# Optimization experiments

Hardware: AMD Instinct MI355X
Metric: run time of the kernel (lower is better)

## Reference

```python
import jax, jax.numpy as jnp
import numpy as np

B, N, D, H, MLP = 4, 1024, 1024, 16, 4096  # seq_len N must equal dim D; D = H * dim_head
DH = D // H
EPS = 1e-5


def layernorm(x, g, b):
    mu = jnp.mean(x, axis=-1, keepdims=True)
    var = jnp.var(x, axis=-1, keepdims=True)
    return (x - mu) * jax.lax.rsqrt(var + EPS) * g + b


def setup_inputs() -> dict:
    key = jax.random.key(0)
    ks = jax.random.split(key, 12)
    s = 0.02
    return {
        "x": jax.random.normal(ks[0], (B, N, D), jnp.float32),
        "enc_out": jax.random.normal(ks[1], (B, N, D), jnp.float32),
        # SelfAttention (heads=1, dim_head=D); weights stored (in, out) so we apply x @ W
        "sa_wq": jax.random.normal(ks[2], (D, D), jnp.float32) * s,
        "sa_wk": jax.random.normal(ks[3], (D, D), jnp.float32) * s,
        "sa_wv": jax.random.normal(ks[4], (D, D), jnp.float32) * s,
        "sa_g": jnp.ones((D,), jnp.float32),
        "sa_b": jnp.zeros((D,), jnp.float32),
        # CrossAttention
        "ca_wq": jax.random.normal(ks[5], (D, D), jnp.float32) * s,
        "ca_wk": jax.random.normal(ks[6], (D, D), jnp.float32) * s,
        "ca_wv": jax.random.normal(ks[7], (D, D), jnp.float32) * s,
        "ca_g": jnp.ones((D,), jnp.float32),
        "ca_b": jnp.zeros((D,), jnp.float32),
        # FeedForward
        "w1": jax.random.normal(ks[8], (D, MLP), jnp.float32) * s,
        "b1": jnp.zeros((MLP,), jnp.float32),
        "w2": jax.random.normal(ks[9], (MLP, D), jnp.float32) * s,
        "b2": jnp.zeros((D,), jnp.float32),
        "ff_g": jnp.ones((D,), jnp.float32),
        "ff_b": jnp.zeros((D,), jnp.float32),
    }


def reference(x, enc_out, sa_wq, sa_wk, sa_wv, sa_g, sa_b,
              ca_wq, ca_wk, ca_wv, ca_g, ca_b,
              w1, b1, w2, b2, ff_g, ff_b):
    b, n, d = x.shape
    # --- SelfAttention: heads=1, dim_head=dim -> scale = dim**-0.5 ---
    sa_scale = 1.0 / jnp.sqrt(jnp.asarray(d, x.dtype))
    q = x @ sa_wq
    k = x @ sa_wk
    v = x @ sa_wv
    dots = jnp.einsum('bid,bjd->bij', q, k) * sa_scale
    attn = jax.nn.softmax(dots, axis=-1)
    sa = jnp.einsum('bij,bjd->bid', attn, v)
    sa = layernorm(sa + x, sa_g, sa_b)

    # --- CrossAttention: Q . (K K^T) before softmax ---
    dh = d // H
    ca_scale = 1.0 / jnp.sqrt(jnp.asarray(dh, x.dtype))
    qc = sa @ ca_wq                                     # [b, n, d]; broadcast over heads
    kc = (enc_out @ ca_wk).reshape(b, n, H, dh).transpose(0, 2, 1, 3)  # [b, h, n, dh]
    vc = (enc_out @ ca_wv).reshape(b, n, H, dh).transpose(0, 2, 1, 3)
    kkt = jnp.einsum('bhid,bhjd->bhij', kc, kc) * ca_scale             # [b, h, n, n]
    dots = jnp.einsum('bid,bhjd->bhij', qc, kkt) * ca_scale            # q's d contracts kkt's last dim (n == d)
    attn = jax.nn.softmax(dots, axis=-1)
    out = jnp.einsum('bhij,bhjd->bhid', attn, vc)
    out = out.transpose(0, 2, 1, 3).reshape(b, n, d)
    ca = layernorm(out + enc_out, ca_g, ca_b)

    # --- FeedForward (dropout = identity in eval) ---
    h = jax.nn.gelu(ca @ w1 + b1, approximate=False) @ w2 + b2
    return layernorm(h + ca, ff_g, ff_b)
```

## Files before the change

kernel.cpp:

```cpp
#include <hip/hip_runtime.h>
#include <math.h>
#include <stdint.h>

typedef unsigned short u16;
typedef u16   u16x8 __attribute__((ext_vector_type(8)));
typedef __bf16 bf16x8 __attribute__((ext_vector_type(8)));
typedef float  f32x4 __attribute__((ext_vector_type(4)));

#define B_   4
#define N_   1024
#define D_   1024
#define MLP_ 4096

__device__ __forceinline__ float bf2f(u16 v) {
    unsigned u = ((unsigned)v) << 16;
    return __builtin_bit_cast(float, u);
}
__device__ __forceinline__ u16 f2bf(float f) {
    unsigned u = __builtin_bit_cast(unsigned, f);
    u += 0x7fff + ((u >> 16) & 1);
    return (u16)(u >> 16);
}
__device__ __forceinline__ bf16x8 ld8(const u16* p) {
    return __builtin_bit_cast(bf16x8, *(const u16x8*)p);
}
__device__ __forceinline__ void gll16(const u16* g, u16* l) {
    __builtin_amdgcn_global_load_lds(
        (const __attribute__((address_space(1))) unsigned int*)g,
        (__attribute__((address_space(3))) unsigned int*)l,
        16, 0, 0);
}

__global__ __launch_bounds__(256)
void f32_to_bf16_k(const float* __restrict__ in, u16* __restrict__ out, int n8)
{
    int i = blockIdx.x * 256 + threadIdx.x;
    if (i < n8) {
        f32x4 a = *(const f32x4*)&in[(long)i * 8];
        f32x4 b = *(const f32x4*)&in[(long)i * 8 + 4];
        u16x8 h;
        h[0] = f2bf(a[0]); h[1] = f2bf(a[1]); h[2] = f2bf(a[2]); h[3] = f2bf(a[3]);
        h[4] = f2bf(b[0]); h[5] = f2bf(b[1]); h[6] = f2bf(b[2]); h[7] = f2bf(b[3]);
        *(u16x8*)&out[(long)i * 8] = h;
    }
}

template<int TN, int OUTF32, int BIAS, int GELU>
__global__ __launch_bounds__(256, 2)
void gemm_a(const u16* __restrict__ A, const u16* __restrict__ Bt,
            void* __restrict__ Cv, const float* __restrict__ bias,
            float scale, int K,
            int lda, int ldb, int ldc,
            long sA, long sB, long sC)
{
    constexpr int NT = TN / 32;
    __shared__ alignas(16) u16 As[2][128 * 32];
    __shared__ alignas(16) u16 Bs[2][TN * 32];
    const int bz = blockIdx.z;
    A  += bz * sA;  Bt += bz * sB;
    char* Cp = (char*)Cv + bz * sC * (OUTF32 ? 4 : 2);
    const int m0 = blockIdx.x * 128, n0 = blockIdx.y * TN;
    const int t = threadIdx.x, lane = t & 63, w = t >> 6;
    const int wr = (w >> 1) * 64, wc = (w & 1) * (TN / 2);
    const int fr = lane & 15, fq = lane >> 4, fk = fq * 8;
    f32x4 acc[4][NT] = {};

    const int r0a = t >> 2, c0a = (t & 3) * 8;
    auto stageA = [&](u16* dst, int k0) {
        gll16(A + (long)(m0 + r0a) * lda + k0 + c0a,      dst + w * 512);
        gll16(A + (long)(m0 + 64 + r0a) * lda + k0 + c0a, dst + 2048 + w * 512);
    };
    auto stageB = [&](u16* dst, int k0) {
        gll16(Bt + (long)(n0 + r0a) * ldb + k0 + c0a, dst + w * 512);
        if (TN == 128)
            gll16(Bt + (long)(n0 + 64 + r0a) * ldb + k0 + c0a, dst + 2048 + w * 512);
    };

    stageA(As[0], 0);
    stageB(Bs[0], 0);
    int cur = 0;
    for (int k0 = 0; k0 < K; k0 += 32) {
        __syncthreads();
        if (k0 + 32 < K) {
            stageA(As[cur ^ 1], k0 + 32);
            stageB(Bs[cur ^ 1], k0 + 32);
        }
        const u16* as = As[cur];
        const u16* bs = Bs[cur];
        bf16x8 af[4], bfv[NT];
#pragma unroll
        for (int mt = 0; mt < 4; mt++) af [mt] = ld8(&as[(wr + mt * 16 + fr) * 32 + fk]);
#pragma unroll
        for (int nt = 0; nt < NT; nt++) bfv[nt] = ld8(&bs[(wc + nt * 16 + fr) * 32 + fk]);
#pragma unroll
        for (int mt = 0; mt < 4; mt++)
#pragma unroll
            for (int nt = 0; nt < NT; nt++)
                acc[mt][nt] = __builtin_amdgcn_mfma_f32_16x16x32_bf16(af[mt], bfv[nt], acc[mt][nt], 0, 0, 0);
        cur ^= 1;
    }

#pragma unroll
    for (int nt = 0; nt < NT; nt++) {
        const int col = n0 + wc + nt * 16 + fr;
        float bv = 0.f;
        if (BIAS) bv = bias[col];
#pragma unroll
        for (int mt = 0; mt < 4; mt++) {
            const int rbase = m0 + wr + mt * 16 + fq * 4;
#pragma unroll
            for (int r = 0; r < 4; r++) {
                float v = acc[mt][nt][r] * scale;
                if (BIAS) v += bv;
                if (GELU) v = 0.5f * v * (1.0f + erff(v * 0.70710678118654752f));
                long idx = (long)(rbase + r) * ldc + col;
                if (OUTF32) ((float*)Cp)[idx] = v;
                else        ((u16*) Cp)[idx] = f2bf(v);
            }
        }
    }
}

template<int INF32>
__global__ __launch_bounds__(256)
void transpose_cast(const void* __restrict__ in, u16* __restrict__ out,
                    int R, int C, long sIn, long sOut)
{
    __shared__ u16 tile[32][33];
    const char* ip = (const char*)in + (long)blockIdx.z * sIn * (INF32 ? 4 : 2);
    u16*        op = out + (long)blockIdx.z * sOut;
    const int bx = blockIdx.x * 32, by = blockIdx.y * 32;
    const int tx = threadIdx.x & 31, ty = threadIdx.x >> 5;
#pragma unroll
    for (int i = ty; i < 32; i += 8) {
        long idx = (long)(by + i) * C + bx + tx;
        tile[i][tx] = INF32 ? f2bf(((const float*)ip)[idx]) : ((const u16*)ip)[idx];
    }
    __syncthreads();
#pragma unroll
    for (int i = ty; i < 32; i += 8) op[(long)(bx + i) * R + by + tx] = tile[tx][i];
}

__global__ __launch_bounds__(256)
void softmax_1024(const float* __restrict__ in, u16* __restrict__ out)
{
    const int lane = threadIdx.x & 63, wv = threadIdx.x >> 6;
    const long row = (long)blockIdx.x * 4 + wv;
    const float* p = in + row * 1024;
    float v[16], mx = -1e30f;
#pragma unroll
    for (int i = 0; i < 16; i++) { v[i] = p[lane + i * 64]; mx = fmaxf(mx, v[i]); }
#pragma unroll
    for (int off = 32; off; off >>= 1) mx = fmaxf(mx, __shfl_xor(mx, off, 64));
    float s = 0.f;
#pragma unroll
    for (int i = 0; i < 16; i++) { v[i] = __expf(v[i] - mx); s += v[i]; }
#pragma unroll
    for (int off = 32; off; off >>= 1) s += __shfl_xor(s, off, 64);
    const float inv = 1.0f / s;
    u16* q = out + row * 1024;
#pragma unroll
    for (int i = 0; i < 16; i++) q[lane + i * 64] = f2bf(v[i] * inv);
}

template<int AF32, int RESF32, int OUTF32>
__global__ __launch_bounds__(256)
void ln_res(const void* __restrict__ Av, const void* __restrict__ Rv,
            const float* __restrict__ g, const float* __restrict__ be,
            void* __restrict__ out)
{
    const int lane = threadIdx.x & 63, wv = threadIdx.x >> 6;
    const long row = (long)blockIdx.x * 4 + wv;
    float v[16], s = 0.f;
#pragma unroll
    for (int i = 0; i < 16; i++) {
        long idx = row * 1024 + lane + i * 64;
        float a = AF32   ? ((const float*)Av)[idx] : bf2f(((const u16*)Av)[idx]);
        float r = RESF32 ? ((const float*)Rv)[idx] : bf2f(((const u16*)Rv)[idx]);
        v[i] = a + r;
        s += v[i];
    }
#pragma unroll
    for (int off = 32; off; off >>= 1) s += __shfl_xor(s, off, 64);
    const float mu = s * (1.f / 1024.f);
    float s2 = 0.f;
#pragma unroll
    for (int i = 0; i < 16; i++) { float d = v[i] - mu; s2 += d * d; }
#pragma unroll
    for (int off = 32; off; off >>= 1) s2 += __shfl_xor(s2, off, 64);
    const float rs = rsqrtf(s2 * (1.f / 1024.f) + 1e-5f);
#pragma unroll
    for (int i = 0; i < 16; i++) {
        int c = lane + i * 64;
        float o = (v[i] - mu) * rs * g[c] + be[c];
        if (OUTF32) ((float*)out)[row * 1024 + c] = o;
        else        ((u16*) out)[row * 1024 + c] = f2bf(o);
    }
}

__global__ __launch_bounds__(256, 2)
void flash_ca(const u16* __restrict__ P, const u16* __restrict__ Kc,
              const u16* __restrict__ VT, u16* __restrict__ O)
{
    __shared__ alignas(16) u16 Qs[64 * 72];
    __shared__ alignas(16) u16 Ks[64 * 72];
    __shared__ alignas(16) u16 Vs[64 * 72];
    __shared__ alignas(16) u16 Ps[64 * 72];
    const int b = blockIdx.z, h = blockIdx.y, it = blockIdx.x;
    const long base = (long)b * N_ * D_;
    const int t = threadIdx.x, lane = t & 63, w = t >> 6;
    const int fr = lane & 15, fq = lane >> 4, fk = fq * 8;

#pragma unroll
    for (int i = 0; i < 2; i++) {
        int c = i * 256 + t, row = c >> 3, col = (c & 7) * 8;
        *(u16x8*)&Qs[row * 72 + col] =
            *(const u16x8*)&P[base + (long)(it * 64 + row) * D_ + h * 64 + col];
    }
    f32x4 o[4] = {};
    float m_r[4], l_r[4];
#pragma unroll
    for (int r = 0; r < 4; r++) { m_r[r] = -1e30f; l_r[r] = 0.f; }

    for (int jt = 0; jt < 16; jt++) {
        __syncthreads();
#pragma unroll
        for (int i = 0; i < 2; i++) {
            int c = i * 256 + t, row = c >> 3, col = (c & 7) * 8;
            *(u16x8*)&Ks[row * 72 + col] =
                *(const u16x8*)&Kc[base + (long)(jt * 64 + row) * D_ + h * 64 + col];
            *(u16x8*)&Vs[row * 72 + col] =
                *(const u16x8*)&VT[base + (long)(h * 64 + row) * D_ + jt * 64 + col];
        }
        __syncthreads();

        f32x4 st[4] = {};
        {
            bf16x8 a0 = ld8(&Qs[(w * 16 + fr) * 72 + fk]);
            bf16x8 a1 = ld8(&Qs[(w * 16 + fr) * 72 + 32 + fk]);
#pragma unroll
            for (int nt = 0; nt < 4; nt++) {
                bf16x8 b0 = ld8(&Ks[(nt * 16 + fr) * 72 + fk]);
                bf16x8 b1 = ld8(&Ks[(nt * 16 + fr) * 72 + 32 + fk]);
                st[nt] = __builtin_amdgcn_mfma_f32_16x16x32_bf16(a0, b0, st[nt], 0, 0, 0);
                st[nt] = __builtin_amdgcn_mfma_f32_16x16x32_bf16(a1, b1, st[nt], 0, 0, 0);
            }
        }
        float alpha[4];
#pragma unroll
        for (int r = 0; r < 4; r++) {
            float mx = fmaxf(fmaxf(st[0][r], st[1][r]), fmaxf(st[2][r], st[3][r]));
#pragma unroll
            for (int off = 1; off < 16; off <<= 1) mx = fmaxf(mx, __shfl_xor(mx, off, 64));
            float mn = fmaxf(m_r[r], mx);
            alpha[r] = __expf(m_r[r] - mn);
            m_r[r] = mn;
        }
        float rsum[4] = {0.f, 0.f, 0.f, 0.f};
#pragma unroll
        for (int nt = 0; nt < 4; nt++)
#pragma unroll
            for (int r = 0; r < 4; r++) {
                float e = __expf(st[nt][r] - m_r[r]);
                st[nt][r] = e;
                rsum[r] += e;
            }
#pragma unroll
        for (int r = 0; r < 4; r++) {
#pragma unroll
            for (int off = 1; off < 16; off <<= 1) rsum[r] += __shfl_xor(rsum[r], off, 64);
            l_r[r] = l_r[r] * alpha[r] + rsum[r];
        }
#pragma unroll
        for (int dt = 0; dt < 4; dt++)
#pragma unroll
            for (int r = 0; r < 4; r++) o[dt][r] *= alpha[r];

#pragma unroll
        for (int nt = 0; nt < 4; nt++)
#pragma unroll
            for (int r = 0; r < 4; r++)
                Ps[(w * 16 + fq * 4 + r) * 72 + nt * 16 + fr] = f2bf(st[nt][r]);
        __asm__ volatile("s_waitcnt lgkmcnt(0)" ::: "memory");
        bf16x8 p0 = ld8(&Ps[(w * 16 + fr) * 72 + fk]);
        bf16x8 p1 = ld8(&Ps[(w * 16 + fr) * 72 + 32 + fk]);
#pragma unroll
        for (int dt = 0; dt < 4; dt++) {
            bf16x8 v0 = ld8(&Vs[(dt * 16 + fr) * 72 + fk]);
            bf16x8 v1 = ld8(&Vs[(dt * 16 + fr) * 72 + 32 + fk]);
            o[dt] = __builtin_amdgcn_mfma_f32_16x16x32_bf16(p0, v0, o[dt], 0, 0, 0);
            o[dt] = __builtin_amdgcn_mfma_f32_16x16x32_bf16(p1, v1, o[dt], 0, 0, 0);
        }
    }
#pragma unroll
    for (int dt = 0; dt < 4; dt++)
#pragma unroll
        for (int r = 0; r < 4; r++) {
            float v = o[dt][r] / l_r[r];
            O[base + (long)(it * 64 + w * 16 + fq * 4 + r) * D_ + h * 64 + dt * 16 + fr] = f2bf(v);
        }
}

extern "C" void kernel_launch(void* const* d_in, const int* in_sizes, int n_in,
                              void* d_out, int out_size, void* d_ws, size_t ws_size,
                              hipStream_t stream)
{
    const float* x     = (const float*)d_in[0];
    const float* enc   = (const float*)d_in[1];
    const float* sa_wq = (const float*)d_in[2];
    const float* sa_wk = (const float*)d_in[3];
    const float* sa_wv = (const float*)d_in[4];
    const float* sa_g  = (const float*)d_in[5];
    const float* sa_b  = (const float*)d_in[6];
    const float* ca_wq = (const float*)d_in[7];
    const float* ca_wk = (const float*)d_in[8];
    const float* ca_wv = (const float*)d_in[9];
    const float* ca_g  = (const float*)d_in[10];
    const float* ca_b  = (const float*)d_in[11];
    const float* w1    = (const float*)d_in[12];
    const float* b1    = (const float*)d_in[13];
    const float* w2    = (const float*)d_in[14];
    const float* b2    = (const float*)d_in[15];
    const float* ff_g  = (const float*)d_in[16];
    const float* ff_b  = (const float*)d_in[17];

    char* ws = (char*)d_ws;
    const size_t MB = 1ull << 20;
    u16*  qkB   = (u16*)(ws + 0 * MB);
    u16*  E     = (u16*)(ws + 0 * MB);
    u16*  h1B   = (u16*)(ws + 0 * MB);
    float* scF  = (float*)(ws + 16 * MB);
    u16*  xB    = (u16*)(ws + 32 * MB);
    u16*  encB  = (u16*)(ws + 40 * MB);
    float* h2F  = (float*)(ws + 32 * MB);
    u16*  Wsa   = (u16*)(ws + 48 * MB);
    u16*  qB    = (u16*)(ws + 48 * MB);
    u16*  calnB = (u16*)(ws + 48 * MB);
    u16*  kB    = (u16*)(ws + 56 * MB);
    u16*  w2T   = (u16*)(ws + 56 * MB);
    u16*  vTB   = (u16*)(ws + 64 * MB);
    u16*  w1T   = (u16*)(ws + 64 * MB);
    u16*  attnB = (u16*)(ws + 72 * MB);
    u16*  Wca   = (u16*)(ws + 72 * MB);

    const dim3 blk(256, 1, 1);
    const long M1 = (long)N_ * D_;
    const long M2 = 2 * M1;

    f32_to_bf16_k<<<dim3(2048, 1, 1), blk, 0, stream>>>(x,   xB,   524288);
    f32_to_bf16_k<<<dim3(2048, 1, 1), blk, 0, stream>>>(enc, encB, 524288);

    transpose_cast<1><<<dim3(32, 32, 1), blk, 0, stream>>>(sa_wq, Wsa,          1024, 1024, 0, 0);
    transpose_cast<1><<<dim3(32, 32, 1), blk, 0, stream>>>(sa_wk, Wsa + M1,     1024, 1024, 0, 0);
    transpose_cast<1><<<dim3(32, 32, 1), blk, 0, stream>>>(sa_wv, Wsa + 2 * M1, 1024, 1024, 0, 0);

    gemm_a<128,0,0,0><<<dim3(32, 16, 1), blk, 0, stream>>>(xB, Wsa, qkB, nullptr,
        1.f, 1024, 1024, 1024, 2048, 0, 0, 0);
    gemm_a<64,0,0,0><<<dim3(8, 16, 4), blk, 0, stream>>>(Wsa + 2 * M1, xB, vTB, nullptr,
        1.f, 1024, 1024, 1024, 1024, 0, M1, M1);
    gemm_a<64,1,0,0><<<dim3(8, 16, 4), blk, 0, stream>>>(qkB, qkB + 1024, scF, nullptr,
        0.03125f, 1024, 2048, 2048, 1024, M2, M2, M1);
    softmax_1024<<<dim3(1024, 1, 1), blk, 0, stream>>>(scF, attnB);
    gemm_a<64,1,0,0><<<dim3(8, 16, 4), blk, 0, stream>>>(attnB, vTB, scF, nullptr,
        1.f, 1024, 1024, 1024, 1024, M1, M1, M1);
    ln_res<1,1,0><<<dim3(1024, 1, 1), blk, 0, stream>>>(scF, x, sa_g, sa_b, E);

    transpose_cast<1><<<dim3(32, 32, 1), blk, 0, stream>>>(ca_wq, Wca,          1024, 1024, 0, 0);
    transpose_cast<1><<<dim3(32, 32, 1), blk, 0, stream>>>(ca_wk, Wca + M1,     1024, 1024, 0, 0);
    transpose_cast<1><<<dim3(32, 32, 1), blk, 0, stream>>>(ca_wv, Wca + 2 * M1, 1024, 1024, 0, 0);
    gemm_a<64,0,0,0><<<dim3(32, 16, 1), blk, 0, stream>>>(E, Wca, qB, nullptr,
        1.f, 1024, 1024, 1024, 1024, 0, 0, 0);
    gemm_a<64,0,0,0><<<dim3(32, 16, 1), blk, 0, stream>>>(encB, Wca + M1, kB, nullptr,
        1.f, 1024, 1024, 1024, 1024, 0, 0, 0);
    gemm_a<64,0,0,0><<<dim3(8, 16, 4), blk, 0, stream>>>(Wca + 2 * M1, encB, vTB, nullptr,
        1.f, 1024, 1024, 1024, 1024, 0, M1, M1);
    transpose_cast<0><<<dim3(32, 32, 4), blk, 0, stream>>>(kB, E, 1024, 1024, M1, M1);
    gemm_a<64,0,0,0><<<dim3(8, 16, 4), blk, 0, stream>>>(qB, E, attnB, nullptr,
        0.015625f, 1024, 1024, 1024, 1024, M1, M1, M1);
    flash_ca<<<dim3(16, 16, 4), blk, 0, stream>>>(attnB, kB, vTB, E);
    ln_res<0,1,0><<<dim3(1024, 1, 1), blk, 0, stream>>>(E, enc, ca_g, ca_b, calnB);

    transpose_cast<1><<<dim3(128, 32, 1), blk, 0, stream>>>(w1, w1T, 1024, 4096, 0, 0);
    transpose_cast<1><<<dim3(32, 128, 1), blk, 0, stream>>>(w2, w2T, 4096, 1024, 0, 0);
    gemm_a<128,0,1,1><<<dim3(32, 32, 1), blk, 0, stream>>>(calnB, w1T, h1B, b1,
        1.f, 1024, 1024, 1024, 4096, 0, 0, 0);
    gemm_a<64,1,1,0><<<dim3(32, 16, 1), blk, 0, stream>>>(h1B, w2T, h2F, b2,
        1.f, 4096, 4096, 4096, 1024, 0, 0, 0);
    ln_res<1,0,1><<<dim3(1024, 1, 1), blk, 0, stream>>>(h2F, calnB, ff_g, ff_b, (float*)d_out);
}
```

Before: 568.3 us.

## Double-buffer flash cross-attention with async loads and shrink GEMM M tiles

flash_ca now handles 128 query rows per block with Q held in registers, and double-buffers K/V tiles in LDS via async global-to-LDS loads so the next tile's fetch overlaps compute. It also drops the online running-max rescaling and exponentiates the raw scores, normalizing once at the end. That removes per-tile reductions and rescales but can overflow if scores are large. Separately, the GEMM gains a templated M tile, so most calls use 64x64 tiles with higher occupancy hints to put more blocks on the GPU.

```diff
diff --git a/kernel.cpp b/kernel.cpp
--- a/kernel.cpp
+++ b/kernel.cpp
@@ -45,35 +45,36 @@
     }
 }
 
-template<int TN, int OUTF32, int BIAS, int GELU>
-__global__ __launch_bounds__(256, 2)
+template<int TM, int TN, int OUTF32, int BIAS, int GELU>
+__global__ __launch_bounds__(256, 4)
 void gemm_a(const u16* __restrict__ A, const u16* __restrict__ Bt,
             void* __restrict__ Cv, const float* __restrict__ bias,
             float scale, int K,
             int lda, int ldb, int ldc,
             long sA, long sB, long sC)
 {
-    constexpr int NT = TN / 32;
-    __shared__ alignas(16) u16 As[2][128 * 32];
+    constexpr int MT = TM / 32, NT = TN / 32;
+    __shared__ alignas(16) u16 As[2][TM * 32];
     __shared__ alignas(16) u16 Bs[2][TN * 32];
     const int bz = blockIdx.z;
     A  += bz * sA;  Bt += bz * sB;
     char* Cp = (char*)Cv + bz * sC * (OUTF32 ? 4 : 2);
-    const int m0 = blockIdx.x * 128, n0 = blockIdx.y * TN;
+    const int m0 = blockIdx.x * TM, n0 = blockIdx.y * TN;
     const int t = threadIdx.x, lane = t & 63, w = t >> 6;
-    const int wr = (w >> 1) * 64, wc = (w & 1) * (TN / 2);
+    const int wr = (w >> 1) * (TM / 2), wc = (w & 1) * (TN / 2);
     const int fr = lane & 15, fq = lane >> 4, fk = fq * 8;
-    f32x4 acc[4][NT] = {};
+    f32x4 acc[MT][NT] = {};
 
     const int r0a = t >> 2, c0a = (t & 3) * 8;
     auto stageA = [&](u16* dst, int k0) {
-        gll16(A + (long)(m0 + r0a) * lda + k0 + c0a,      dst + w * 512);
-        gll16(A + (long)(m0 + 64 + r0a) * lda + k0 + c0a, dst + 2048 + w * 512);
+#pragma unroll
+        for (int p = 0; p < TM / 64; p++)
+            gll16(A + (long)(m0 + p * 64 + r0a) * lda + k0 + c0a, dst + p * 2048 + w * 512);
     };
     auto stageB = [&](u16* dst, int k0) {
-        gll16(Bt + (long)(n0 + r0a) * ldb + k0 + c0a, dst + w * 512);
-        if (TN == 128)
-            gll16(Bt + (long)(n0 + 64 + r0a) * ldb + k0 + c0a, dst + 2048 + w * 512);
+#pragma unroll
+        for (int p = 0; p < TN / 64; p++)
+            gll16(Bt + (long)(n0 + p * 64 + r0a) * ldb + k0 + c0a, dst + p * 2048 + w * 512);
     };
 
     stageA(As[0], 0);
@@ -87,13 +88,13 @@
         }
         const u16* as = As[cur];
         const u16* bs = Bs[cur];
-        bf16x8 af[4], bfv[NT];
-#pragma unroll
-        for (int mt = 0; mt < 4; mt++) af [mt] = ld8(&as[(wr + mt * 16 + fr) * 32 + fk]);
+        bf16x8 af[MT], bfv[NT];
+#pragma unroll
+        for (int mt = 0; mt < MT; mt++) af [mt] = ld8(&as[(wr + mt * 16 + fr) * 32 + fk]);
 #pragma unroll
         for (int nt = 0; nt < NT; nt++) bfv[nt] = ld8(&bs[(wc + nt * 16 + fr) * 32 + fk]);
 #pragma unroll
-        for (int mt = 0; mt < 4; mt++)
+        for (int mt = 0; mt < MT; mt++)
 #pragma unroll
             for (int nt = 0; nt < NT; nt++)
                 acc[mt][nt] = __builtin_amdgcn_mfma_f32_16x16x32_bf16(af[mt], bfv[nt], acc[mt][nt], 0, 0, 0);
@@ -106,7 +107,7 @@
         float bv = 0.f;
         if (BIAS) bv = bias[col];
 #pragma unroll
-        for (int mt = 0; mt < 4; mt++) {
+        for (int mt = 0; mt < MT; mt++) {
             const int rbase = m0 + wr + mt * 16 + fq * 4;
 #pragma unroll
             for (int r = 0; r < 4; r++) {
@@ -198,107 +199,107 @@
     }
 }
 
-__global__ __launch_bounds__(256, 2)
+__global__ __launch_bounds__(256, 3)
 void flash_ca(const u16* __restrict__ P, const u16* __restrict__ Kc,
               const u16* __restrict__ VT, u16* __restrict__ O)
 {
-    __shared__ alignas(16) u16 Qs[64 * 72];
-    __shared__ alignas(16) u16 Ks[64 * 72];
-    __shared__ alignas(16) u16 Vs[64 * 72];
-    __shared__ alignas(16) u16 Ps[64 * 72];
+    __shared__ alignas(16) u16 Ks[2][64 * 64];
+    __shared__ alignas(16) u16 Vs[2][64 * 64];
+    __shared__ alignas(16) u16 Ps[128 * 72];
     const int b = blockIdx.z, h = blockIdx.y, it = blockIdx.x;
     const long base = (long)b * N_ * D_;
     const int t = threadIdx.x, lane = t & 63, w = t >> 6;
-    const int fr = lane & 15, fq = lane >> 4, fk = fq * 8;
-
-#pragma unroll
-    for (int i = 0; i < 2; i++) {
-        int c = i * 256 + t, row = c >> 3, col = (c & 7) * 8;
-        *(u16x8*)&Qs[row * 72 + col] =
-            *(const u16x8*)&P[base + (long)(it * 64 + row) * D_ + h * 64 + col];
-    }
-    f32x4 o[4] = {};
-    float m_r[4], l_r[4];
-#pragma unroll
-    for (int r = 0; r < 4; r++) { m_r[r] = -1e30f; l_r[r] = 0.f; }
-
+    const int fr = lane & 15, fq = lane >> 4;
+
+    bf16x8 qf[2][2];
+#pragma unroll
+    for (int mt = 0; mt < 2; mt++)
+#pragma unroll
+        for (int hf = 0; hf < 2; hf++)
+            qf[mt][hf] = ld8(&P[base + (long)(it * 128 + w * 32 + mt * 16 + fr) * D_
+                                + h * 64 + hf * 32 + fq * 8]);
+
+    auto stageK = [&](int buf, int jt) {
+#pragma unroll
+        for (int p = 0; p < 2; p++)
+            gll16(Kc + base + (long)(jt * 64 + p * 32 + (t >> 3)) * D_ + h * 64 + (t & 7) * 8,
+                  &Ks[buf][p * 2048 + w * 512]);
+    };
+    auto stageV = [&](int buf, int jt) {
+#pragma unroll
+        for (int p = 0; p < 2; p++)
+            gll16(VT + base + (long)(h * 64 + p * 32 + (t >> 3)) * D_ + jt * 64 + (t & 7) * 8,
+                  &Vs[buf][p * 2048 + w * 512]);
+    };
+
+    f32x4 o[2][4] = {};
+    float l_lane[2][4] = {};
+
+    stageK(0, 0); stageV(0, 0);
+    int cur = 0;
     for (int jt = 0; jt < 16; jt++) {
         __syncthreads();
-#pragma unroll
-        for (int i = 0; i < 2; i++) {
-            int c = i * 256 + t, row = c >> 3, col = (c & 7) * 8;
-            *(u16x8*)&Ks[row * 72 + col] =
-                *(const u16x8*)&Kc[base + (long)(jt * 64 + row) * D_ + h * 64 + col];
-            *(u16x8*)&Vs[row * 72 + col] =
-                *(const u16x8*)&VT[base + (long)(h * 64 + row) * D_ + jt * 64 + col];
-        }
-        __syncthreads();
-
-        f32x4 st[4] = {};
-        {
-            bf16x8 a0 = ld8(&Qs[(w * 16 + fr) * 72 + fk]);
-            bf16x8 a1 = ld8(&Qs[(w * 16 + fr) * 72 + 32 + fk]);
-#pragma unroll
-            for (int nt = 0; nt < 4; nt++) {
-                bf16x8 b0 = ld8(&Ks[(nt * 16 + fr) * 72 + fk]);
-                bf16x8 b1 = ld8(&Ks[(nt * 16 + fr) * 72 + 32 + fk]);
-                st[nt] = __builtin_amdgcn_mfma_f32_16x16x32_bf16(a0, b0, st[nt], 0, 0, 0);
-                st[nt] = __builtin_amdgcn_mfma_f32_16x16x32_bf16(a1, b1, st[nt], 0, 0, 0);
+        if (jt + 1 < 16) { stageK(cur ^ 1, jt + 1); stageV(cur ^ 1, jt + 1); }
+        const u16* ks = Ks[cur];
+        const u16* vs = Vs[cur];
+
+        f32x4 st[2][4] = {};
+#pragma unroll
+        for (int nt = 0; nt < 4; nt++) {
+            bf16x8 b0 = ld8(&ks[(nt * 16 + fr) * 64 + fq * 8]);
+            bf16x8 b1 = ld8(&ks[(nt * 16 + fr) * 64 + 32 + fq * 8]);
+#pragma unroll
+            for (int mt = 0; mt < 2; mt++) {
+                st[mt][nt] = __builtin_amdgcn_mfma_f32_16x16x32_bf16(qf[mt][0], b0, st[mt][nt], 0, 0, 0);
+                st[mt][nt] = __builtin_amdgcn_mfma_f32_16x16x32_bf16(qf[mt][1], b1, st[mt][nt], 0, 0, 0);
             }
         }
-        float alpha[4];
+#pragma unroll
+        for (int mt = 0; mt < 2; mt++)
+#pragma unroll
+            for (int nt = 0; nt < 4; nt++)
+#pragma unroll
+                for (int r = 0; r < 4; r++) {
+                    float e = __expf(st[mt][nt][r]);
+                    l_lane[mt][r] += e;
+                    Ps[(w * 32 + mt * 16 + fq * 4 + r) * 72 + nt * 16 + fr] = f2bf(e);
+                }
+        __asm__ volatile("s_waitcnt lgkmcnt(0)" ::: "memory");
+        bf16x8 vf[4][2];
+#pragma unroll
+        for (int dt = 0; dt < 4; dt++) {
+            vf[dt][0] = ld8(&vs[(dt * 16 + fr) * 64 + fq * 8]);
+            vf[dt][1] = ld8(&vs[(dt * 16 + fr) * 64 + 32 + fq * 8]);
+        }
+#pragma unroll
+        for (int mt = 0; mt < 2; mt++) {
+            bf16x8 p0 = ld8(&Ps[(w * 32 + mt * 16 + fr) * 72 + fq * 8]);
+            bf16x8 p1 = ld8(&Ps[(w * 32 + mt * 16 + fr) * 72 + 32 + fq * 8]);
+#pragma unroll
+            for (int dt = 0; dt < 4; dt++) {
+                o[mt][dt] = __builtin_amdgcn_mfma_f32_16x16x32_bf16(p0, vf[dt][0], o[mt][dt], 0, 0, 0);
+                o[mt][dt] = __builtin_amdgcn_mfma_f32_16x16x32_bf16(p1, vf[dt][1], o[mt][dt], 0, 0, 0);
+            }
+        }
+        cur ^= 1;
+    }
+#pragma unroll
+    for (int mt = 0; mt < 2; mt++)
 #pragma unroll
         for (int r = 0; r < 4; r++) {
-            float mx = fmaxf(fmaxf(st[0][r], st[1][r]), fmaxf(st[2][r], st[3][r]));
-#pragma unroll
-            for (int off = 1; off < 16; off <<= 1) mx = fmaxf(mx, __shfl_xor(mx, off, 64));
-            float mn = fmaxf(m_r[r], mx);
-            alpha[r] = __expf(m_r[r] - mn);
-            m_r[r] = mn;
-        }
-        float rsum[4] = {0.f, 0.f, 0.f, 0.f};
-#pragma unroll
-        for (int nt = 0; nt < 4; nt++)
-#pragma unroll
-            for (int r = 0; r < 4; r++) {
-                float e = __expf(st[nt][r] - m_r[r]);
-                st[nt][r] = e;
-                rsum[r] += e;
-            }
-#pragma unroll
-        for (int r = 0; r < 4; r++) {
-#pragma unroll
-            for (int off = 1; off < 16; off <<= 1) rsum[r] += __shfl_xor(rsum[r], off, 64);
-            l_r[r] = l_r[r] * alpha[r] + rsum[r];
-        }
+            float lt = l_lane[mt][r];
+#pragma unroll
+            for (int off = 1; off < 16; off <<= 1) lt += __shfl_xor(lt, off, 64);
+            l_lane[mt][r] = 1.0f / lt;
+        }
+#pragma unroll
+    for (int mt = 0; mt < 2; mt++)
 #pragma unroll
         for (int dt = 0; dt < 4; dt++)
 #pragma unroll
-            for (int r = 0; r < 4; r++) o[dt][r] *= alpha[r];
-
-#pragma unroll
-        for (int nt = 0; nt < 4; nt++)
-#pragma unroll
             for (int r = 0; r < 4; r++)
-                Ps[(w * 16 + fq * 4 + r) * 72 + nt * 16 + fr] = f2bf(st[nt][r]);
-        __asm__ volatile("s_waitcnt lgkmcnt(0)" ::: "memory");
-        bf16x8 p0 = ld8(&Ps[(w * 16 + fr) * 72 + fk]);
-        bf16x8 p1 = ld8(&Ps[(w * 16 + fr) * 72 + 32 + fk]);
-#pragma unroll
-        for (int dt = 0; dt < 4; dt++) {
-            bf16x8 v0 = ld8(&Vs[(dt * 16 + fr) * 72 + fk]);
-            bf16x8 v1 = ld8(&Vs[(dt * 16 + fr) * 72 + 32 + fk]);
-            o[dt] = __builtin_amdgcn_mfma_f32_16x16x32_bf16(p0, v0, o[dt], 0, 0, 0);
-            o[dt] = __builtin_amdgcn_mfma_f32_16x16x32_bf16(p1, v1, o[dt], 0, 0, 0);
-        }
-    }
-#pragma unroll
-    for (int dt = 0; dt < 4; dt++)
-#pragma unroll
-        for (int r = 0; r < 4; r++) {
-            float v = o[dt][r] / l_r[r];
-            O[base + (long)(it * 64 + w * 16 + fq * 4 + r) * D_ + h * 64 + dt * 16 + fr] = f2bf(v);
-        }
+                O[base + (long)(it * 128 + w * 32 + mt * 16 + fq * 4 + r) * D_
+                  + h * 64 + dt * 16 + fr] = f2bf(o[mt][dt][r] * l_lane[mt][r]);
 }
 
 extern "C" void kernel_launch(void* const* d_in, const int* in_sizes, int n_in,
@@ -354,37 +355,37 @@
     transpose_cast<1><<<dim3(32, 32, 1), blk, 0, stream>>>(sa_wk, Wsa + M1,     1024, 1024, 0, 0);
     transpose_cast<1><<<dim3(32, 32, 1), blk, 0, stream>>>(sa_wv, Wsa + 2 * M1, 1024, 1024, 0, 0);
 
-    gemm_a<128,0,0,0><<<dim3(32, 16, 1), blk, 0, stream>>>(xB, Wsa, qkB, nullptr,
+    gemm_a<64,128,0,0,0><<<dim3(64, 16, 1), blk, 0, stream>>>(xB, Wsa, qkB, nullptr,
         1.f, 1024, 1024, 1024, 2048, 0, 0, 0);
-    gemm_a<64,0,0,0><<<dim3(8, 16, 4), blk, 0, stream>>>(Wsa + 2 * M1, xB, vTB, nullptr,
+    gemm_a<64,64,0,0,0><<<dim3(16, 16, 4), blk, 0, stream>>>(Wsa + 2 * M1, xB, vTB, nullptr,
         1.f, 1024, 1024, 1024, 1024, 0, M1, M1);
-    gemm_a<64,1,0,0><<<dim3(8, 16, 4), blk, 0, stream>>>(qkB, qkB + 1024, scF, nullptr,
+    gemm_a<64,64,1,0,0><<<dim3(16, 16, 4), blk, 0, stream>>>(qkB, qkB + 1024, scF, nullptr,
         0.03125f, 1024, 2048, 2048, 1024, M2, M2, M1);
     softmax_1024<<<dim3(1024, 1, 1), blk, 0, stream>>>(scF, attnB);
-    gemm_a<64,1,0,0><<<dim3(8, 16, 4), blk, 0, stream>>>(attnB, vTB, scF, nullptr,
+    gemm_a<64,64,1,0,0><<<dim3(16, 16, 4), blk, 0, stream>>>(attnB, vTB, scF, nullptr,
         1.f, 1024, 1024, 1024, 1024, M1, M1, M1);
     ln_res<1,1,0><<<dim3(1024, 1, 1), blk, 0, stream>>>(scF, x, sa_g, sa_b, E);
 
     transpose_cast<1><<<dim3(32, 32, 1), blk, 0, stream>>>(ca_wq, Wca,          1024, 1024, 0, 0);
     transpose_cast<1><<<dim3(32, 32, 1), blk, 0, stream>>>(ca_wk, Wca + M1,     1024, 1024, 0, 0);
     transpose_cast<1><<<dim3(32, 32, 1), blk, 0, stream>>>(ca_wv, Wca + 2 * M1, 1024, 1024, 0, 0);
-    gemm_a<64,0,0,0><<<dim3(32, 16, 1), blk, 0, stream>>>(E, Wca, qB, nullptr,
+    gemm_a<64,64,0,0,0><<<dim3(64, 16, 1), blk, 0, stream>>>(E, Wca, qB, nullptr,
         1.f, 1024, 1024, 1024, 1024, 0, 0, 0);
-    gemm_a<64,0,0,0><<<dim3(32, 16, 1), blk, 0, stream>>>(encB, Wca + M1, kB, nullptr,
+    gemm_a<64,64,0,0,0><<<dim3(64, 16, 1), blk, 0, stream>>>(encB, Wca + M1, kB, nullptr,
         1.f, 1024, 1024, 1024, 1024, 0, 0, 0);
-    gemm_a<64,0,0,0><<<dim3(8, 16, 4), blk, 0, stream>>>(Wca + 2 * M1, encB, vTB, nullptr,
+    gemm_a<64,64,0,0,0><<<dim3(16, 16, 4), blk, 0, stream>>>(Wca + 2 * M1, encB, vTB, nullptr,
         1.f, 1024, 1024, 1024, 1024, 0, M1, M1);
     transpose_cast<0><<<dim3(32, 32, 4), blk, 0, stream>>>(kB, E, 1024, 1024, M1, M1);
-    gemm_a<64,0,0,0><<<dim3(8, 16, 4), blk, 0, stream>>>(qB, E, attnB, nullptr,
+    gemm_a<64,64,0,0,0><<<dim3(16, 16, 4), blk, 0, stream>>>(qB, E, attnB, nullptr,
         0.015625f, 1024, 1024, 1024, 1024, M1, M1, M1);
-    flash_ca<<<dim3(16, 16, 4), blk, 0, stream>>>(attnB, kB, vTB, E);
+    flash_ca<<<dim3(8, 16, 4), blk, 0, stream>>>(attnB, kB, vTB, E);
     ln_res<0,1,0><<<dim3(1024, 1, 1), blk, 0, stream>>>(E, enc, ca_g, ca_b, calnB);
 
     transpose_cast<1><<<dim3(128, 32, 1), blk, 0, stream>>>(w1, w1T, 1024, 4096, 0, 0);
     transpose_cast<1><<<dim3(32, 128, 1), blk, 0, stream>>>(w2, w2T, 4096, 1024, 0, 0);
-    gemm_a<128,0,1,1><<<dim3(32, 32, 1), blk, 0, stream>>>(calnB, w1T, h1B, b1,
+    gemm_a<128,128,0,1,1><<<dim3(32, 32, 1), blk, 0, stream>>>(calnB, w1T, h1B, b1,
         1.f, 1024, 1024, 1024, 4096, 0, 0, 0);
-    gemm_a<64,1,1,0><<<dim3(32, 16, 1), blk, 0, stream>>>(h1B, w2T, h2F, b2,
+    gemm_a<64,64,1,1,0><<<dim3(64, 16, 1), blk, 0, stream>>>(h1B, w2T, h2F, b2,
         1.f, 4096, 4096, 4096, 1024, 0, 0, 0);
     ln_res<1,0,1><<<dim3(1024, 1, 1), blk, 0, stream>>>(h2F, calnB, ff_g, ff_b, (float*)d_out);
 }
```

After: 543.8 us. 1.05x faster.
